# Kernel tuning notes

Measured on AMD Instinct MI355X. Metric: run time of the kernel, lower is better.

Reference implementation:

```python
import jax, jax.numpy as jnp
import numpy as np
from jax.scipy.special import logsumexp

N, C, D = 400000, 256, 3


def setup_inputs() -> dict:
    key = jax.random.key(0)
    k1, k2 = jax.random.split(key)
    X = jax.random.normal(k1, (N, D), dtype=jnp.float32)
    mu = jax.random.normal(k2, (C, D), dtype=jnp.float32)
    w = jnp.zeros((C,), dtype=jnp.float32)
    # sigma as in __init__: 0.1 * (r / C**(1/D)), r = sqrt(sum of per-dim variances of mu)
    r = jnp.sqrt(jnp.var(mu, axis=0).sum())
    sigma = (0.1 * (r / C ** (1.0 / D)))[None].astype(jnp.float32)
    return {"X": X, "mu": mu, "w": w, "sigma": sigma}


def reference(X, mu, w, sigma):
    """One EM step of the uniform-covariance GMM (no outliers). Returns (Y, Cfe)."""
    n, d = X.shape
    sig = sigma[0]
    # E-step: squared distances (N,C) and log-responsibilities
    D2_nc = jnp.sum((X[:, None, :] - mu[None, :, :]) ** 2, axis=-1)  # (N,C)
    loggaussnorm = d * (jnp.log(sig) + 0.5 * jnp.log(2.0 * jnp.pi))
    Zw = logsumexp(w)
    t_nc = w[None, :] - Zw - D2_nc / (2.0 * sig ** 2) - loggaussnorm  # (N,C)
    T_n = logsumexp(t_nc, axis=1)
    lgamma_nc = t_nc - T_n[:, None]
    gamma_nc = jnp.exp(lgamma_nc)
    # M-step updates (order matters, as in the torch code)
    mu_new = jax.nn.softmax(lgamma_nc, axis=0).T @ X            # (C,D)
    w_new = logsumexp(lgamma_nc, axis=0)                        # (C,)
    sig_new = jnp.sqrt(jnp.sum(gamma_nc * D2_nc) / (d * n))     # scalar
    # Quadratic targets Y_n = sum_c gamma_nc * mu_c (with updated mu)
    Y = gamma_nc @ mu_new                                       # (N,D)
    # Free-energy offset (loggaussnorm uses OLD sigma; 1/(2 sigma^2) uses NEW sigma)
    lpi_c = w_new - logsumexp(w_new)
    Cfe = jnp.sum(
        gamma_nc
        * (
            (jnp.sum(mu_new ** 2, axis=-1)[None, :] - jnp.sum(Y ** 2, axis=-1)[:, None])
            / (2.0 * sig_new ** 2)
            + loggaussnorm
            + lgamma_nc
            - lpi_c[None, :]
        )
    )
    return Y, Cfe
```

## Files before the change

### kernel.cpp

```cpp
#include <hip/hip_runtime.h>
#include <math.h>

#define CC   256
#define TILE 256

#define OFF_P     0
#define OFF_Q     1024
#define OFF_S     2048
#define OFF_CD    3072
#define OFF_CF    3080
#define OFF_T2    3088

__device__ __forceinline__ float fexp2(float x) { return __builtin_amdgcn_exp2f(x); }
__device__ __forceinline__ float flog2(float x) { return __builtin_amdgcn_logf(x); }

__global__ __launch_bounds__(256) void gmm_prep(const float* __restrict__ mu,
                                                const float* __restrict__ w,
                                                const float* __restrict__ sigma,
                                                float* __restrict__ ws)
{
    __shared__ float redA[4], redB[4];
    const int c = threadIdx.x;
    const int lane = c & 63, wid = c >> 6;

    ws[OFF_S + c] = 0.f; ws[OFF_S + 256 + c] = 0.f;
    ws[OFF_S + 512 + c] = 0.f; ws[OFF_S + 768 + c] = 0.f;
    if (c < 4) ((double*)(ws + OFF_CD))[c] = 0.0;
    if (c >= 8 && c < 16) ws[OFF_CF + (c - 6)] = 0.f;

    float wc = w[c];
    float m = wc;
    #pragma unroll
    for (int off = 32; off > 0; off >>= 1) m = fmaxf(m, __shfl_xor(m, off));
    if (lane == 0) redA[wid] = m;
    __syncthreads();
    m = fmaxf(fmaxf(redA[0], redA[1]), fmaxf(redA[2], redA[3]));
    float e = expf(wc - m);
    #pragma unroll
    for (int off = 32; off > 0; off >>= 1) e += __shfl_xor(e, off);
    if (lane == 0) redB[wid] = e;
    __syncthreads();
    float Zw = m + logf(redB[0] + redB[1] + redB[2] + redB[3]);

    const float L = 1.4426950408889634f;
    float sig = sigma[0];
    float lgn = 3.0f * (logf(sig) + 0.91893853320467274f);
    float k = L / (2.0f * sig * sig);
    float twok = 2.0f * k;
    float mx = mu[3*c], my = mu[3*c+1], mz = mu[3*c+2];
    float m2 = mx*mx + my*my + mz*mz;
    float alpha = (wc - Zw - lgn) * L - k * m2;
    ((float4*)(ws + OFF_P))[c] = make_float4(twok*mx, twok*my, twok*mz, alpha);
    if (c == 0) { ws[OFF_CF + 0] = twok; ws[OFF_CF + 1] = lgn; }
}

__global__ __launch_bounds__(256) void gmm_pass1(const float* __restrict__ X,
                                                 float* __restrict__ ws, int N)
{
    __shared__ float4 Psh[CC];
    __shared__ float4 XT[TILE];
    __shared__ float2 msP[2][TILE];
    __shared__ float4 Bpart[CC];
    __shared__ double redd[2][4];

    const int tid  = threadIdx.x;
    const int pi   = tid & 127;
    const int half = tid >> 7;
    const int n0   = blockIdx.x * TILE;
    const int NT   = min(TILE, N - n0);

    Psh[tid] = ((const float4*)(ws + OFF_P))[tid];

    const int i0 = pi, i1 = pi + 128;
    const bool v0 = i0 < NT, v1 = i1 < NT;
    float x0=0.f,y0=0.f,z0=0.f, x1=0.f,y1=0.f,z1=0.f;
    if (v0) { const float* p = X + 3*(size_t)(n0+i0); x0=p[0]; y0=p[1]; z0=p[2]; }
    if (v1) { const float* p = X + 3*(size_t)(n0+i1); x1=p[0]; y1=p[1]; z1=p[2]; }
    float q0 = fmaf(x0,x0, fmaf(y0,y0, z0*z0));
    float q1 = fmaf(x1,x1, fmaf(y1,y1, z1*z1));
    __syncthreads();

    const float4* Pc = Psh + half*128;
    float m0=-3.0e38f, m1=-3.0e38f, s0=0.f, s1=0.f;
    for (int c0 = 0; c0 < 128; c0 += 8) {
        float u0[8], u1[8];
        #pragma unroll
        for (int j = 0; j < 8; ++j) {
            float4 p = Pc[c0 + j];
            u0[j] = fmaf(x0,p.x, fmaf(y0,p.y, fmaf(z0,p.z, p.w)));
            u1[j] = fmaf(x1,p.x, fmaf(y1,p.y, fmaf(z1,p.z, p.w)));
        }
        float a0 = fmaxf(fmaxf(u0[0],u0[1]), fmaxf(u0[2],u0[3]));
        float b0 = fmaxf(fmaxf(u0[4],u0[5]), fmaxf(u0[6],u0[7]));
        float M0 = fmaxf(a0, b0);
        float a1 = fmaxf(fmaxf(u1[0],u1[1]), fmaxf(u1[2],u1[3]));
        float b1 = fmaxf(fmaxf(u1[4],u1[5]), fmaxf(u1[6],u1[7]));
        float M1 = fmaxf(a1, b1);
        if (__any((M0 > m0) || (M1 > m1))) {
            M0 = fmaxf(M0, m0); M1 = fmaxf(M1, m1);
            s0 *= fexp2(m0 - M0);
            s1 *= fexp2(m1 - M1);
            m0 = M0; m1 = M1;
        }
        #pragma unroll
        for (int j = 0; j < 8; ++j) {
            s0 += fexp2(u0[j] - m0);
            s1 += fexp2(u1[j] - m1);
        }
    }
    msP[half][i0] = make_float2(m0, s0);
    msP[half][i1] = make_float2(m1, s1);
    __syncthreads();

    double xd = 0.0, td = 0.0;
    if (half == 0) {
        if (v0) {
            float2 a = msP[0][i0], b = msP[1][i0];
            float M = fmaxf(a.x, b.x);
            float T2 = M + flog2(a.y*fexp2(a.x-M) + b.y*fexp2(b.x-M));
            XT[i0] = make_float4(x0,y0,z0,T2);
            ws[OFF_T2 + n0 + i0] = T2;
            xd += (double)q0; td += (double)T2;
        }
        if (v1) {
            float2 a = msP[0][i1], b = msP[1][i1];
            float M = fmaxf(a.x, b.x);
            float T2 = M + flog2(a.y*fexp2(a.x-M) + b.y*fexp2(b.x-M));
            XT[i1] = make_float4(x1,y1,z1,T2);
            ws[OFF_T2 + n0 + i1] = T2;
            xd += (double)q1; td += (double)T2;
        }
    }
    {
        const int lane = tid & 63, wid = tid >> 6;
        #pragma unroll
        for (int off = 32; off > 0; off >>= 1) { xd += __shfl_xor(xd, off); td += __shfl_xor(td, off); }
        if (lane == 0) { redd[0][wid] = xd; redd[1][wid] = td; }
    }
    __syncthreads();
    if (tid == 0) {
        double* CD = (double*)(ws + OFF_CD);
        atomicAdd(CD + 0, redd[0][0]+redd[0][1]+redd[0][2]+redd[0][3]);
        atomicAdd(CD + 1, redd[1][0]+redd[1][1]+redd[1][2]+redd[1][3]);
    }

    float4 pA = Psh[pi], pB = Psh[pi + 128];
    float SA=0.f,AxA=0.f,AyA=0.f,AzA=0.f, SB=0.f,AxB=0.f,AyB=0.f,AzB=0.f;
    const int nlo = half*128, nhi = min(nlo+128, NT);
    #pragma unroll 8
    for (int n = nlo; n < nhi; ++n) {
        float4 xt = XT[n];
        float uA = fmaf(xt.x,pA.x, fmaf(xt.y,pA.y, fmaf(xt.z,pA.z, pA.w)));
        float uB = fmaf(xt.x,pB.x, fmaf(xt.y,pB.y, fmaf(xt.z,pB.z, pB.w)));
        float gA = fexp2(uA - xt.w);
        float gB = fexp2(uB - xt.w);
        SA+=gA; AxA=fmaf(gA,xt.x,AxA); AyA=fmaf(gA,xt.y,AyA); AzA=fmaf(gA,xt.z,AzA);
        SB+=gB; AxB=fmaf(gB,xt.x,AxB); AyB=fmaf(gB,xt.y,AyB); AzB=fmaf(gB,xt.z,AzB);
    }
    if (half == 1) {
        Bpart[pi]       = make_float4(SA,AxA,AyA,AzA);
        Bpart[pi + 128] = make_float4(SB,AxB,AyB,AzB);
    }
    __syncthreads();
    if (half == 0) {
        float4 bA = Bpart[pi], bB = Bpart[pi + 128];
        SA+=bA.x; AxA+=bA.y; AyA+=bA.z; AzA+=bA.w;
        SB+=bB.x; AxB+=bB.y; AyB+=bB.z; AzB+=bB.w;
        float* Sg = ws + OFF_S;
        atomicAdd(Sg       + pi, SA);   atomicAdd(Sg       + pi + 128, SB);
        atomicAdd(Sg + 256 + pi, AxA);  atomicAdd(Sg + 256 + pi + 128, AxB);
        atomicAdd(Sg + 512 + pi, AyA);  atomicAdd(Sg + 512 + pi + 128, AyB);
        atomicAdd(Sg + 768 + pi, AzA);  atomicAdd(Sg + 768 + pi + 128, AzB);
    }
}

__global__ __launch_bounds__(256) void gmm_pass2(float* __restrict__ ws, int N)
{
    __shared__ double red6[6][4];
    const int c = threadIdx.x;
    const int lane = c & 63, wid = c >> 6;
    const float twok = ws[OFF_CF + 0];
    const double invt = 1.0 / (double)twok;
    double* CD = (double*)(ws + OFF_CD);

    float Sc  = ws[OFF_S       + c];
    float Axc = ws[OFF_S + 256 + c];
    float Ayc = ws[OFF_S + 512 + c];
    float Azc = ws[OFF_S + 768 + c];
    float4 p  = ((const float4*)(ws + OFF_P))[c];

    float inv = 1.0f / fmaxf(Sc, 1e-37f);
    float mx = Axc * inv, my = Ayc * inv, mz = Azc * inv;
    ((float4*)(ws + OFF_Q))[c] = make_float4(mx, my, mz, 0.f);

    double v0 = (double)Sc;
    double v1 = (double)Sc * (double)(mx*mx + my*my + mz*mz);
    double v2 = (double)Sc * log((double)fmaxf(Sc, 1e-37f));
    double v3 = (double)Sc * (double)(p.x*p.x + p.y*p.y + p.z*p.z);
    double v4 = (double)Sc * (double)p.w;
    double v5 = (double)(p.x*Axc + p.y*Ayc + p.z*Azc);

    #pragma unroll
    for (int off = 32; off > 0; off >>= 1) {
        v0 += __shfl_xor(v0, off); v1 += __shfl_xor(v1, off); v2 += __shfl_xor(v2, off);
        v3 += __shfl_xor(v3, off); v4 += __shfl_xor(v4, off); v5 += __shfl_xor(v5, off);
    }
    if (lane == 0) { red6[0][wid]=v0; red6[1][wid]=v1; red6[2][wid]=v2;
                     red6[3][wid]=v3; red6[4][wid]=v4; red6[5][wid]=v5; }
    __syncthreads();
    if (c == 0) {
        double sumS   = red6[0][0]+red6[0][1]+red6[0][2]+red6[0][3];
        double sumSM2 = red6[1][0]+red6[1][1]+red6[1][2]+red6[1][3];
        double sumSlS = red6[2][0]+red6[2][1]+red6[2][2]+red6[2][3];
        double sumMSs = red6[3][0]+red6[3][1]+red6[3][2]+red6[3][3];
        double sumAS  = red6[4][0]+red6[4][1]+red6[4][2]+red6[4][3];
        double dotMAs = red6[5][0]+red6[5][1]+red6[5][2]+red6[5][3];
        double sumX2  = CD[0];
        double sumT2  = CD[1];
        double sumGD2 = sumX2 + sumMSs*invt*invt - 2.0 * dotMAs*invt;
        double sn2    = sumGD2 / (3.0 * (double)N);
        ws[OFF_CF + 2] = (float)(1.0 / (2.0 * sn2));
        ws[OFF_CF + 3] = (float)(sumSlS - sumS * log(sumS));
        ws[OFF_CF + 4] = (float)(sumAS + dotMAs - sumT2);
        CD[3] = sumSM2;
    }
}

__global__ __launch_bounds__(256) void gmm_pass3(const float* __restrict__ X,
                                                 float* __restrict__ ws,
                                                 float* __restrict__ out, int N)
{
    __shared__ float4 Psh[CC], Qsh[CC];
    __shared__ float4 Yp[2][TILE];
    __shared__ double redd[4];

    const int tid  = threadIdx.x;
    const int pi   = tid & 127;
    const int half = tid >> 7;
    const int n0   = blockIdx.x * TILE;
    const int NT   = min(TILE, N - n0);

    Psh[tid] = ((const float4*)(ws + OFF_P))[tid];
    Qsh[tid] = ((const float4*)(ws + OFF_Q))[tid];

    const int i0 = pi, i1 = pi + 128;
    const bool v0 = i0 < NT, v1 = i1 < NT;
    float x0=0.f,y0=0.f,z0=0.f,T0=0.f, x1=0.f,y1=0.f,z1=0.f,T1=0.f;
    if (v0) { const float* p = X + 3*(size_t)(n0+i0); x0=p[0]; y0=p[1]; z0=p[2]; T0 = ws[OFF_T2+n0+i0]; }
    if (v1) { const float* p = X + 3*(size_t)(n0+i1); x1=p[0]; y1=p[1]; z1=p[2]; T1 = ws[OFF_T2+n0+i1]; }
    __syncthreads();

    const float4* Pc = Psh + half*128;
    const float4* Qc = Qsh + half*128;
    float Yx0=0.f,Yy0=0.f,Yz0=0.f, Yx1=0.f,Yy1=0.f,Yz1=0.f;
    #pragma unroll 8
    for (int c = 0; c < 128; ++c) {
        float4 p = Pc[c];
        float u0 = fmaf(x0,p.x, fmaf(y0,p.y, fmaf(z0,p.z, p.w)));
        float u1 = fmaf(x1,p.x, fmaf(y1,p.y, fmaf(z1,p.z, p.w)));
        float g0 = fexp2(u0 - T0);
        float g1 = fexp2(u1 - T1);
        float4 q = Qc[c];
        Yx0 = fmaf(g0,q.x,Yx0); Yy0 = fmaf(g0,q.y,Yy0); Yz0 = fmaf(g0,q.z,Yz0);
        Yx1 = fmaf(g1,q.x,Yx1); Yy1 = fmaf(g1,q.y,Yy1); Yz1 = fmaf(g1,q.z,Yz1);
    }
    Yp[half][i0] = make_float4(Yx0,Yy0,Yz0,0.f);
    Yp[half][i1] = make_float4(Yx1,Yy1,Yz1,0.f);
    __syncthreads();

    double y2d = 0.0;
    if (half == 0) {
        if (v0) {
            float4 a = Yp[0][i0], b = Yp[1][i0];
            float yx = a.x+b.x, yy = a.y+b.y, yz = a.z+b.z;
            float* op = out + 3*(size_t)(n0+i0);
            op[0]=yx; op[1]=yy; op[2]=yz;
            y2d += (double)yx*yx + (double)yy*yy + (double)yz*yz;
        }
        if (v1) {
            float4 a = Yp[0][i1], b = Yp[1][i1];
            float yx = a.x+b.x, yy = a.y+b.y, yz = a.z+b.z;
            float* op = out + 3*(size_t)(n0+i1);
            op[0]=yx; op[1]=yy; op[2]=yz;
            y2d += (double)yx*yx + (double)yy*yy + (double)yz*yz;
        }
    }
    {
        const int lane = tid & 63, wid = tid >> 6;
        #pragma unroll
        for (int off = 32; off > 0; off >>= 1) y2d += __shfl_xor(y2d, off);
        if (lane == 0) redd[wid] = y2d;
    }
    __syncthreads();
    if (tid == 0) atomicAdd(((double*)(ws + OFF_CD)) + 2, redd[0]+redd[1]+redd[2]+redd[3]);
}

__global__ void gmm_pass4(float* __restrict__ ws, float* __restrict__ cfe_out, int N)
{
    if (threadIdx.x == 0) {
        double* CD = (double*)(ws + OFF_CD);
        double Cfe = (CD[3] - CD[2]) * (double)ws[OFF_CF + 2]
                   + (double)N * (double)ws[OFF_CF + 1]
                   + 0.69314718055994531 * (double)ws[OFF_CF + 4]
                   - (double)ws[OFF_CF + 3];
        cfe_out[0] = (float)Cfe;
    }
}

extern "C" void kernel_launch(void* const* d_in, const int* in_sizes, int n_in,
                              void* d_out, int out_size, void* d_ws, size_t ws_size,
                              hipStream_t stream)
{
    const float* X     = (const float*)d_in[0];
    const float* mu    = (const float*)d_in[1];
    const float* w     = (const float*)d_in[2];
    const float* sigma = (const float*)d_in[3];
    float* out = (float*)d_out;
    float* ws  = (float*)d_ws;
    const int N = in_sizes[0] / 3;
    const int nblk = (N + TILE - 1) / TILE;

    gmm_prep <<<1,    256, 0, stream>>>(mu, w, sigma, ws);
    gmm_pass1<<<nblk, 256, 0, stream>>>(X, ws, N);
    gmm_pass2<<<1,    256, 0, stream>>>(ws, N);
    gmm_pass3<<<nblk, 256, 0, stream>>>(X, ws, out, N);
    gmm_pass4<<<1,    64,  0, stream>>>(ws, out + (size_t)3 * N, N);
}
```

Baseline: 94.32 us.

## Remove pass2 launch by computing means in pass3 and folding scalars into pass4

Drops the single-block pass2 kernel. Each pass3 block now recomputes the new means from the accumulated sums, and the scalar reductions move into the final pass4 kernel, which computes Cfe directly. Pass1's logsumexp loop is widened to 16 components per step with split accumulators, and pass1 gets a minimum-occupancy launch bound. This saves one kernel launch and its serialization gap, at the cost of redundant per-block division work and possible register pressure in pass1.

```diff
diff --git a/kernel.cpp b/kernel.cpp
--- a/kernel.cpp
+++ b/kernel.cpp
@@ -26,7 +26,6 @@
     ws[OFF_S + c] = 0.f; ws[OFF_S + 256 + c] = 0.f;
     ws[OFF_S + 512 + c] = 0.f; ws[OFF_S + 768 + c] = 0.f;
     if (c < 4) ((double*)(ws + OFF_CD))[c] = 0.0;
-    if (c >= 8 && c < 16) ws[OFF_CF + (c - 6)] = 0.f;
 
     float wc = w[c];
     float m = wc;
@@ -54,8 +53,8 @@
     if (c == 0) { ws[OFF_CF + 0] = twok; ws[OFF_CF + 1] = lgn; }
 }
 
-__global__ __launch_bounds__(256) void gmm_pass1(const float* __restrict__ X,
-                                                 float* __restrict__ ws, int N)
+__global__ __launch_bounds__(256, 4) void gmm_pass1(const float* __restrict__ X,
+                                                    float* __restrict__ ws, int N)
 {
     __shared__ float4 Psh[CC];
     __shared__ float4 XT[TILE];
@@ -81,35 +80,45 @@
     __syncthreads();
 
     const float4* Pc = Psh + half*128;
-    float m0=-3.0e38f, m1=-3.0e38f, s0=0.f, s1=0.f;
-    for (int c0 = 0; c0 < 128; c0 += 8) {
-        float u0[8], u1[8];
+    float m0=-3.0e38f, m1=-3.0e38f;
+    float s0a=0.f, s0b=0.f, s1a=0.f, s1b=0.f;
+    for (int c0 = 0; c0 < 128; c0 += 16) {
+        float u0[16], u1[16];
         #pragma unroll
-        for (int j = 0; j < 8; ++j) {
+        for (int j = 0; j < 16; ++j) {
             float4 p = Pc[c0 + j];
             u0[j] = fmaf(x0,p.x, fmaf(y0,p.y, fmaf(z0,p.z, p.w)));
             u1[j] = fmaf(x1,p.x, fmaf(y1,p.y, fmaf(z1,p.z, p.w)));
         }
-        float a0 = fmaxf(fmaxf(u0[0],u0[1]), fmaxf(u0[2],u0[3]));
-        float b0 = fmaxf(fmaxf(u0[4],u0[5]), fmaxf(u0[6],u0[7]));
-        float M0 = fmaxf(a0, b0);
-        float a1 = fmaxf(fmaxf(u1[0],u1[1]), fmaxf(u1[2],u1[3]));
-        float b1 = fmaxf(fmaxf(u1[4],u1[5]), fmaxf(u1[6],u1[7]));
-        float M1 = fmaxf(a1, b1);
+        float M0, M1;
+        {
+            float a = fmaxf(fmaxf(u0[0],u0[1]), fmaxf(u0[2],u0[3]));
+            float b = fmaxf(fmaxf(u0[4],u0[5]), fmaxf(u0[6],u0[7]));
+            float c = fmaxf(fmaxf(u0[8],u0[9]), fmaxf(u0[10],u0[11]));
+            float d = fmaxf(fmaxf(u0[12],u0[13]), fmaxf(u0[14],u0[15]));
+            M0 = fmaxf(fmaxf(a,b), fmaxf(c,d));
+            a = fmaxf(fmaxf(u1[0],u1[1]), fmaxf(u1[2],u1[3]));
+            b = fmaxf(fmaxf(u1[4],u1[5]), fmaxf(u1[6],u1[7]));
+            c = fmaxf(fmaxf(u1[8],u1[9]), fmaxf(u1[10],u1[11]));
+            d = fmaxf(fmaxf(u1[12],u1[13]), fmaxf(u1[14],u1[15]));
+            M1 = fmaxf(fmaxf(a,b), fmaxf(c,d));
+        }
         if (__any((M0 > m0) || (M1 > m1))) {
             M0 = fmaxf(M0, m0); M1 = fmaxf(M1, m1);
-            s0 *= fexp2(m0 - M0);
-            s1 *= fexp2(m1 - M1);
+            float r0 = fexp2(m0 - M0), r1 = fexp2(m1 - M1);
+            s0a *= r0; s0b *= r0; s1a *= r1; s1b *= r1;
             m0 = M0; m1 = M1;
         }
         #pragma unroll
-        for (int j = 0; j < 8; ++j) {
-            s0 += fexp2(u0[j] - m0);
-            s1 += fexp2(u1[j] - m1);
-        }
-    }
-    msP[half][i0] = make_float2(m0, s0);
-    msP[half][i1] = make_float2(m1, s1);
+        for (int j = 0; j < 16; j += 2) {
+            s0a += fexp2(u0[j]   - m0);
+            s0b += fexp2(u0[j+1] - m0);
+            s1a += fexp2(u1[j]   - m1);
+            s1b += fexp2(u1[j+1] - m1);
+        }
+    }
+    msP[half][i0] = make_float2(m0, s0a + s0b);
+    msP[half][i1] = make_float2(m1, s1a + s1b);
     __syncthreads();
 
     double xd = 0.0, td = 0.0;
@@ -174,58 +183,6 @@
     }
 }
 
-__global__ __launch_bounds__(256) void gmm_pass2(float* __restrict__ ws, int N)
-{
-    __shared__ double red6[6][4];
-    const int c = threadIdx.x;
-    const int lane = c & 63, wid = c >> 6;
-    const float twok = ws[OFF_CF + 0];
-    const double invt = 1.0 / (double)twok;
-    double* CD = (double*)(ws + OFF_CD);
-
-    float Sc  = ws[OFF_S       + c];
-    float Axc = ws[OFF_S + 256 + c];
-    float Ayc = ws[OFF_S + 512 + c];
-    float Azc = ws[OFF_S + 768 + c];
-    float4 p  = ((const float4*)(ws + OFF_P))[c];
-
-    float inv = 1.0f / fmaxf(Sc, 1e-37f);
-    float mx = Axc * inv, my = Ayc * inv, mz = Azc * inv;
-    ((float4*)(ws + OFF_Q))[c] = make_float4(mx, my, mz, 0.f);
-
-    double v0 = (double)Sc;
-    double v1 = (double)Sc * (double)(mx*mx + my*my + mz*mz);
-    double v2 = (double)Sc * log((double)fmaxf(Sc, 1e-37f));
-    double v3 = (double)Sc * (double)(p.x*p.x + p.y*p.y + p.z*p.z);
-    double v4 = (double)Sc * (double)p.w;
-    double v5 = (double)(p.x*Axc + p.y*Ayc + p.z*Azc);
-
-    #pragma unroll
-    for (int off = 32; off > 0; off >>= 1) {
-        v0 += __shfl_xor(v0, off); v1 += __shfl_xor(v1, off); v2 += __shfl_xor(v2, off);
-        v3 += __shfl_xor(v3, off); v4 += __shfl_xor(v4, off); v5 += __shfl_xor(v5, off);
-    }
-    if (lane == 0) { red6[0][wid]=v0; red6[1][wid]=v1; red6[2][wid]=v2;
-                     red6[3][wid]=v3; red6[4][wid]=v4; red6[5][wid]=v5; }
-    __syncthreads();
-    if (c == 0) {
-        double sumS   = red6[0][0]+red6[0][1]+red6[0][2]+red6[0][3];
-        double sumSM2 = red6[1][0]+red6[1][1]+red6[1][2]+red6[1][3];
-        double sumSlS = red6[2][0]+red6[2][1]+red6[2][2]+red6[2][3];
-        double sumMSs = red6[3][0]+red6[3][1]+red6[3][2]+red6[3][3];
-        double sumAS  = red6[4][0]+red6[4][1]+red6[4][2]+red6[4][3];
-        double dotMAs = red6[5][0]+red6[5][1]+red6[5][2]+red6[5][3];
-        double sumX2  = CD[0];
-        double sumT2  = CD[1];
-        double sumGD2 = sumX2 + sumMSs*invt*invt - 2.0 * dotMAs*invt;
-        double sn2    = sumGD2 / (3.0 * (double)N);
-        ws[OFF_CF + 2] = (float)(1.0 / (2.0 * sn2));
-        ws[OFF_CF + 3] = (float)(sumSlS - sumS * log(sumS));
-        ws[OFF_CF + 4] = (float)(sumAS + dotMAs - sumT2);
-        CD[3] = sumSM2;
-    }
-}
-
 __global__ __launch_bounds__(256) void gmm_pass3(const float* __restrict__ X,
                                                  float* __restrict__ ws,
                                                  float* __restrict__ out, int N)
@@ -241,7 +198,14 @@
     const int NT   = min(TILE, N - n0);
 
     Psh[tid] = ((const float4*)(ws + OFF_P))[tid];
-    Qsh[tid] = ((const float4*)(ws + OFF_Q))[tid];
+    {
+        float Sc  = ws[OFF_S       + tid];
+        float Axc = ws[OFF_S + 256 + tid];
+        float Ayc = ws[OFF_S + 512 + tid];
+        float Azc = ws[OFF_S + 768 + tid];
+        float inv = 1.0f / fmaxf(Sc, 1e-37f);
+        Qsh[tid] = make_float4(Axc*inv, Ayc*inv, Azc*inv, 0.f);
+    }
 
     const int i0 = pi, i1 = pi + 128;
     const bool v0 = i0 < NT, v1 = i1 < NT;
@@ -295,14 +259,59 @@
     if (tid == 0) atomicAdd(((double*)(ws + OFF_CD)) + 2, redd[0]+redd[1]+redd[2]+redd[3]);
 }
 
-__global__ void gmm_pass4(float* __restrict__ ws, float* __restrict__ cfe_out, int N)
-{
-    if (threadIdx.x == 0) {
-        double* CD = (double*)(ws + OFF_CD);
-        double Cfe = (CD[3] - CD[2]) * (double)ws[OFF_CF + 2]
-                   + (double)N * (double)ws[OFF_CF + 1]
-                   + 0.69314718055994531 * (double)ws[OFF_CF + 4]
-                   - (double)ws[OFF_CF + 3];
+__global__ __launch_bounds__(256) void gmm_pass4(float* __restrict__ ws,
+                                                 float* __restrict__ cfe_out, int N)
+{
+    __shared__ double red6[6][4];
+    const int c = threadIdx.x;
+    const int lane = c & 63, wid = c >> 6;
+    const float twok = ws[OFF_CF + 0];
+    const double invt = 1.0 / (double)twok;
+    double* CD = (double*)(ws + OFF_CD);
+
+    float Sc  = ws[OFF_S       + c];
+    float Axc = ws[OFF_S + 256 + c];
+    float Ayc = ws[OFF_S + 512 + c];
+    float Azc = ws[OFF_S + 768 + c];
+    float4 p  = ((const float4*)(ws + OFF_P))[c];
+
+    float inv = 1.0f / fmaxf(Sc, 1e-37f);
+    float mx = Axc * inv, my = Ayc * inv, mz = Azc * inv;
+
+    double v0 = (double)Sc;
+    double v1 = (double)Sc * (double)(mx*mx + my*my + mz*mz);
+    double v2 = (double)Sc * log((double)fmaxf(Sc, 1e-37f));
+    double v3 = (double)Sc * (double)(p.x*p.x + p.y*p.y + p.z*p.z);
+    double v4 = (double)Sc * (double)p.w;
+    double v5 = (double)(p.x*Axc + p.y*Ayc + p.z*Azc);
+
+    #pragma unroll
+    for (int off = 32; off > 0; off >>= 1) {
+        v0 += __shfl_xor(v0, off); v1 += __shfl_xor(v1, off); v2 += __shfl_xor(v2, off);
+        v3 += __shfl_xor(v3, off); v4 += __shfl_xor(v4, off); v5 += __shfl_xor(v5, off);
+    }
+    if (lane == 0) { red6[0][wid]=v0; red6[1][wid]=v1; red6[2][wid]=v2;
+                     red6[3][wid]=v3; red6[4][wid]=v4; red6[5][wid]=v5; }
+    __syncthreads();
+    if (c == 0) {
+        double sumS   = red6[0][0]+red6[0][1]+red6[0][2]+red6[0][3];
+        double sumSM2 = red6[1][0]+red6[1][1]+red6[1][2]+red6[1][3];
+        double sumSlS = red6[2][0]+red6[2][1]+red6[2][2]+red6[2][3];
+        double sumMSs = red6[3][0]+red6[3][1]+red6[3][2]+red6[3][3];
+        double sumAS  = red6[4][0]+red6[4][1]+red6[4][2]+red6[4][3];
+        double dotMAs = red6[5][0]+red6[5][1]+red6[5][2]+red6[5][3];
+        double sumX2  = CD[0];
+        double sumT2  = CD[1];
+        double sumY2  = CD[2];
+        double sumGD2 = sumX2 + sumMSs*invt*invt - 2.0 * dotMAs*invt;
+        double sn2    = sumGD2 / (3.0 * (double)N);
+        double sumSlpi = sumSlS - sumS * log(sumS);
+        double sumGL2  = sumAS + dotMAs - sumT2;
+        double lgn     = (double)ws[OFF_CF + 1];
+        double Cfe = (sumSM2 - sumY2) / (2.0 * sn2)
+                   + (double)N * lgn
+                   + 0.69314718055994531 * sumGL2
+                   - sumSlpi;
         cfe_out[0] = (float)Cfe;
     }
 }
@@ -322,7 +331,6 @@
 
     gmm_prep <<<1,    256, 0, stream>>>(mu, w, sigma, ws);
     gmm_pass1<<<nblk, 256, 0, stream>>>(X, ws, N);
-    gmm_pass2<<<1,    256, 0, stream>>>(ws, N);
     gmm_pass3<<<nblk, 256, 0, stream>>>(X, ws, out, N);
-    gmm_pass4<<<1,    64,  0, stream>>>(ws, out + (size_t)3 * N, N);
-}
+    gmm_pass4<<<1,    256, 0, stream>>>(ws, out + (size_t)3 * N, N);
+}
```

Result: faster. 92.29 us (-2.1%).
